# Performance work log

Hardware: AMD Instinct MI355X
Metric: run time of the kernel (lower is better)

## Reference

```python
import jax, jax.numpy as jnp
import numpy as np

N = 8192
IN_DIM = 256
HIDDEN = 128


def setup_inputs() -> dict:
    key = jax.random.key(0)
    k1, k2 = jax.random.split(key)
    X = jax.random.normal(k1, (N, IN_DIM), dtype=jnp.float32)
    # nn.Linear(in_dim, hidden, bias=False): weight [hidden, in_dim]
    W = jax.random.normal(k2, (HIDDEN, IN_DIM), dtype=jnp.float32) * (1.0 / np.sqrt(IN_DIM))
    return {"X": X, "W": W}


def reference(X, W):
    # Z = X @ W.T : [N, hidden]
    Z = jnp.einsum('ni,hi->nh', X, W)
    # Dense similarity graph: ReLU(Z Z^T), row-normalized
    A = jax.nn.relu(jnp.einsum('nh,mh->nm', Z, Z))  # [N, N]
    A = A / (A.sum(axis=-1, keepdims=True) + 1e-6)
    out = jnp.einsum('nm,mh->nh', A, Z)  # [N, hidden]
    return (out, A)
```

## Files before the change

### kernel.cpp

```cpp
#include <hip/hip_runtime.h>


#define NR 8192
#define KD 256
#define HD 128

typedef short v8s __attribute__((ext_vector_type(8)));
typedef float v4f __attribute__((ext_vector_type(4)));

static __device__ __forceinline__ ushort f2bf(float f) {
    union { float f; unsigned u; } c; c.f = f;
    unsigned u = c.u;
    u += 0x7fffu + ((u >> 16) & 1u);
    return (ushort)(u >> 16);
}
static __device__ __forceinline__ float bf2f(ushort b) {
    union { unsigned u; float f; } c; c.u = ((unsigned)b) << 16; return c.f;
}
static __device__ __forceinline__ unsigned pk2(float a, float b) {
    union { float f; unsigned u; } x, y; x.f = a; y.f = b;
    unsigned ua = x.u + 0x7fffu + ((x.u >> 16) & 1u);
    unsigned ub = y.u + 0x7fffu + ((y.u >> 16) & 1u);
    return (ua >> 16) | (ub & 0xffff0000u);
}

__global__ __launch_bounds__(256) void k_z(const float* __restrict__ X,
                                           const float* __restrict__ W,
                                           ushort* __restrict__ Zb,
                                           ushort* __restrict__ ZbT) {
    __shared__ ushort Xhi[16][264];
    __shared__ ushort Xlo[16][264];
    int tid = threadIdx.x, lane = tid & 63, wave = tid >> 6;
    int lm = lane & 15, lq = lane >> 4;
    int n0 = blockIdx.x * 16;
    int hbase = wave * 32;
    v8s Whi[2][8], Wlo[2][8];
#pragma unroll
    for (int hi = 0; hi < 2; ++hi) {
        const float* wp = W + (hbase + hi * 16 + lm) * KD + lq * 8;
#pragma unroll
        for (int ks = 0; ks < 8; ++ks) {
            float4 w0 = *(const float4*)(wp + ks * 32);
            float4 w1 = *(const float4*)(wp + ks * 32 + 4);
            float wv[8] = {w0.x, w0.y, w0.z, w0.w, w1.x, w1.y, w1.z, w1.w};
#pragma unroll
            for (int j = 0; j < 8; ++j) {
                ushort h = f2bf(wv[j]);
                Whi[hi][ks][j] = (short)h;
                Wlo[hi][ks][j] = (short)f2bf(wv[j] - bf2f(h));
            }
        }
    }
#pragma unroll
    for (int t = 0; t < 4; ++t) {
        int idx = tid + t * 256;
        int r = idx >> 6, c4 = (idx & 63) * 4;
        float4 x = *(const float4*)(X + (size_t)(n0 + r) * KD + c4);
        ushort h0 = f2bf(x.x), h1 = f2bf(x.y), h2 = f2bf(x.z), h3 = f2bf(x.w);
        unsigned a = ((unsigned)h0) | ((unsigned)h1 << 16);
        unsigned b = ((unsigned)h2) | ((unsigned)h3 << 16);
        unsigned c = ((unsigned)f2bf(x.x - bf2f(h0))) | ((unsigned)f2bf(x.y - bf2f(h1)) << 16);
        unsigned d = ((unsigned)f2bf(x.z - bf2f(h2))) | ((unsigned)f2bf(x.w - bf2f(h3)) << 16);
        *(uint2*)&Xhi[r][c4] = make_uint2(a, b);
        *(uint2*)&Xlo[r][c4] = make_uint2(c, d);
    }
    __syncthreads();
    {
        v8s Ah[8], Al[8];
#pragma unroll
        for (int ks = 0; ks < 8; ++ks) {
            Ah[ks] = *(const v8s*)&Xhi[lm][ks * 32 + lq * 8];
            Al[ks] = *(const v8s*)&Xlo[lm][ks * 32 + lq * 8];
        }
        v4f acc[2] = {{0.f, 0.f, 0.f, 0.f}, {0.f, 0.f, 0.f, 0.f}};
#pragma unroll
        for (int ks = 0; ks < 8; ++ks)
#pragma unroll
            for (int hi = 0; hi < 2; ++hi) {
                acc[hi] = __builtin_amdgcn_mfma_f32_16x16x32_bf16(Ah[ks], Whi[hi][ks], acc[hi], 0, 0, 0);
                acc[hi] = __builtin_amdgcn_mfma_f32_16x16x32_bf16(Ah[ks], Wlo[hi][ks], acc[hi], 0, 0, 0);
                acc[hi] = __builtin_amdgcn_mfma_f32_16x16x32_bf16(Al[ks], Whi[hi][ks], acc[hi], 0, 0, 0);
            }
#pragma unroll
        for (int hi = 0; hi < 2; ++hi) {
            int h = hbase + hi * 16 + lm;
            int nb = n0 + lq * 4;
            ushort b0 = f2bf(acc[hi][0]), b1 = f2bf(acc[hi][1]);
            ushort b2 = f2bf(acc[hi][2]), b3 = f2bf(acc[hi][3]);
            Zb[(size_t)(nb + 0) * HD + h] = b0;
            Zb[(size_t)(nb + 1) * HD + h] = b1;
            Zb[(size_t)(nb + 2) * HD + h] = b2;
            Zb[(size_t)(nb + 3) * HD + h] = b3;
            *(uint2*)&ZbT[(size_t)h * NR + nb] =
                make_uint2(((unsigned)b0) | ((unsigned)b1 << 16), ((unsigned)b2) | ((unsigned)b3 << 16));
        }
    }
}

__global__ __launch_bounds__(256) void k_rowsum(const ushort* __restrict__ Zb,
                                                float* __restrict__ rowsum) {
    __shared__ ushort ZC[2][64][136];
    int tid = threadIdx.x, lane = tid & 63, wave = tid >> 6;
    int lm = lane & 15, lq = lane >> 4;
    int rb = blockIdx.x >> 4, cs = blockIdx.x & 15;
    int row0 = rb * 128, cstart = cs * 512;
    v8s Bfr[2][4];
#pragma unroll
    for (int ri = 0; ri < 2; ++ri)
#pragma unroll
        for (int ks = 0; ks < 4; ++ks)
            Bfr[ri][ks] =
                *(const v8s*)(Zb + (size_t)(row0 + wave * 32 + ri * 16 + lm) * HD + ks * 32 + lq * 8);
    float rs[2] = {0.f, 0.f};
#pragma unroll
    for (int t = 0; t < 4; ++t) {
        int idx = tid + t * 256;
        int r = idx >> 4, c8 = (idx & 15) * 8;
        *(uint4*)&ZC[0][r][c8] = *(const uint4*)(Zb + (size_t)(cstart + r) * HD + c8);
    }
    __syncthreads();
    for (int it = 0; it < 8; ++it) {
        int cur = it & 1;
        int c0 = cstart + it * 64;
        uint4 sr[4];
        if (it < 7) {
#pragma unroll
            for (int t = 0; t < 4; ++t) {
                int idx = tid + t * 256;
                int r = idx >> 4, c8 = (idx & 15) * 8;
                sr[t] = *(const uint4*)(Zb + (size_t)(c0 + 64 + r) * HD + c8);
            }
        }
#pragma unroll
        for (int ci = 0; ci < 4; ++ci) {
            v8s Af[4];
#pragma unroll
            for (int ks = 0; ks < 4; ++ks)
                Af[ks] = *(const v8s*)&ZC[cur][ci * 16 + lm][ks * 32 + lq * 8];
            v4f a0 = {0.f, 0.f, 0.f, 0.f}, a1 = {0.f, 0.f, 0.f, 0.f};
#pragma unroll
            for (int ks = 0; ks < 4; ++ks) {
                a0 = __builtin_amdgcn_mfma_f32_16x16x32_bf16(Af[ks], Bfr[0][ks], a0, 0, 0, 0);
                a1 = __builtin_amdgcn_mfma_f32_16x16x32_bf16(Af[ks], Bfr[1][ks], a1, 0, 0, 0);
            }
            rs[0] += fmaxf(a0[0], 0.f) + fmaxf(a0[1], 0.f) + fmaxf(a0[2], 0.f) + fmaxf(a0[3], 0.f);
            rs[1] += fmaxf(a1[0], 0.f) + fmaxf(a1[1], 0.f) + fmaxf(a1[2], 0.f) + fmaxf(a1[3], 0.f);
        }
        if (it < 7) {
#pragma unroll
            for (int t = 0; t < 4; ++t) {
                int idx = tid + t * 256;
                int r = idx >> 4, c8 = (idx & 15) * 8;
                *(uint4*)&ZC[cur ^ 1][r][c8] = sr[t];
            }
        }
        __syncthreads();
    }
#pragma unroll
    for (int ri = 0; ri < 2; ++ri) {
        float v = rs[ri];
        v += __shfl_xor(v, 16, 64);
        v += __shfl_xor(v, 32, 64);
        if (lq == 0) atomicAdd(&rowsum[row0 + wave * 32 + ri * 16 + lm], v);
    }
}

__global__ __launch_bounds__(256) void k_main(const ushort* __restrict__ Zb,
                                              const ushort* __restrict__ ZbT,
                                              const float* __restrict__ rowsum,
                                              float* __restrict__ outp,
                                              float* __restrict__ Ap) {
    __shared__ ushort ZC[2][64][136];
    __shared__ ushort PT[2][64][72];
    int tid = threadIdx.x, lane = tid & 63, wave = tid >> 6;
    int lm = lane & 15, lq = lane >> 4;
    int rb = blockIdx.x >> 3, cs = blockIdx.x & 7;
    int row0 = rb * 64, colb = cs * 1024;
    int wr2 = wave >> 1, wc2 = wave & 1;
    v8s Bfr[2][4];
#pragma unroll
    for (int ri = 0; ri < 2; ++ri)
#pragma unroll
        for (int ks = 0; ks < 4; ++ks)
            Bfr[ri][ks] =
                *(const v8s*)(Zb + (size_t)(row0 + wr2 * 32 + ri * 16 + lm) * HD + ks * 32 + lq * 8);
    float rsv[2];
#pragma unroll
    for (int ri = 0; ri < 2; ++ri)
        rsv[ri] = 1.0f / (rowsum[row0 + wr2 * 32 + ri * 16 + lm] + 1e-6f);
    v4f U[2][4];
#pragma unroll
    for (int ri = 0; ri < 2; ++ri)
#pragma unroll
        for (int hi = 0; hi < 4; ++hi) U[ri][hi] = (v4f){0.f, 0.f, 0.f, 0.f};

#pragma unroll
    for (int t = 0; t < 4; ++t) {
        int idx = tid + t * 256;
        int r = idx >> 4, c8 = (idx & 15) * 8;
        *(uint4*)&ZC[0][r][c8] = *(const uint4*)(Zb + (size_t)(colb + r) * HD + c8);
    }
    __syncthreads();

    float* ap0 = Ap + (size_t)(row0 + wr2 * 32 + lm) * NR + colb + wc2 * 32 + lq * 4;
    float* ap1 = ap0 + (size_t)16 * NR;

    for (int it = 0; it < 16; ++it) {
        int cur = it & 1;
        int c0 = colb + it * 64;
        uint4 sr[4];
        if (it < 15) {
#pragma unroll
            for (int t = 0; t < 4; ++t) {
                int idx = tid + t * 256;
                int r = idx >> 4, c8 = (idx & 15) * 8;
                sr[t] = *(const uint4*)(Zb + (size_t)(c0 + 64 + r) * HD + c8);
            }
        }
        v8s Bz[4][2];
#pragma unroll
        for (int hi = 0; hi < 4; ++hi)
#pragma unroll
            for (int ks = 0; ks < 2; ++ks)
                Bz[hi][ks] = *(const v8s*)(ZbT + (size_t)(wc2 * 64 + hi * 16 + lm) * NR + c0 +
                                           ks * 32 + lq * 8);
        v4f avst[2][2];
#pragma unroll
        for (int ci = 0; ci < 2; ++ci) {
            v8s Af[4];
#pragma unroll
            for (int ks = 0; ks < 4; ++ks)
                Af[ks] = *(const v8s*)&ZC[cur][wc2 * 32 + ci * 16 + lm][ks * 32 + lq * 8];
            v4f S0 = {0.f, 0.f, 0.f, 0.f}, S1 = {0.f, 0.f, 0.f, 0.f};
#pragma unroll
            for (int ks = 0; ks < 4; ++ks) {
                S0 = __builtin_amdgcn_mfma_f32_16x16x32_bf16(Af[ks], Bfr[0][ks], S0, 0, 0, 0);
                S1 = __builtin_amdgcn_mfma_f32_16x16x32_bf16(Af[ks], Bfr[1][ks], S1, 0, 0, 0);
            }
            int cb = wc2 * 32 + ci * 16 + lq * 4;
            {
                v4f av;
                av[0] = fmaxf(S0[0], 0.f) * rsv[0]; av[1] = fmaxf(S0[1], 0.f) * rsv[0];
                av[2] = fmaxf(S0[2], 0.f) * rsv[0]; av[3] = fmaxf(S0[3], 0.f) * rsv[0];
                avst[ci][0] = av;
                *(uint2*)&PT[cur][wr2 * 32 + lm][cb] = make_uint2(pk2(av[0], av[1]), pk2(av[2], av[3]));
            }
            {
                v4f av;
                av[0] = fmaxf(S1[0], 0.f) * rsv[1]; av[1] = fmaxf(S1[1], 0.f) * rsv[1];
                av[2] = fmaxf(S1[2], 0.f) * rsv[1]; av[3] = fmaxf(S1[3], 0.f) * rsv[1];
                avst[ci][1] = av;
                *(uint2*)&PT[cur][wr2 * 32 + 16 + lm][cb] =
                    make_uint2(pk2(av[0], av[1]), pk2(av[2], av[3]));
            }
        }
        if (it < 15) {
#pragma unroll
            for (int t = 0; t < 4; ++t) {
                int idx = tid + t * 256;
                int r = idx >> 4, c8 = (idx & 15) * 8;
                *(uint4*)&ZC[cur ^ 1][r][c8] = sr[t];
            }
        }
        __syncthreads();
#pragma unroll
        for (int ci = 0; ci < 2; ++ci) {
            __builtin_nontemporal_store(avst[ci][0], (v4f*)(ap0 + ci * 16));
            __builtin_nontemporal_store(avst[ci][1], (v4f*)(ap1 + ci * 16));
        }
#pragma unroll
        for (int ks = 0; ks < 2; ++ks) {
            v8s P0 = *(const v8s*)&PT[cur][wr2 * 32 + lm][ks * 32 + lq * 8];
            v8s P1 = *(const v8s*)&PT[cur][wr2 * 32 + 16 + lm][ks * 32 + lq * 8];
#pragma unroll
            for (int hi = 0; hi < 4; ++hi) {
                U[0][hi] = __builtin_amdgcn_mfma_f32_16x16x32_bf16(P0, Bz[hi][ks], U[0][hi], 0, 0, 0);
                U[1][hi] = __builtin_amdgcn_mfma_f32_16x16x32_bf16(P1, Bz[hi][ks], U[1][hi], 0, 0, 0);
            }
        }
        ap0 += 64;
        ap1 += 64;
    }
#pragma unroll
    for (int ri = 0; ri < 2; ++ri)
#pragma unroll
        for (int hi = 0; hi < 4; ++hi)
#pragma unroll
            for (int j = 0; j < 4; ++j)
                atomicAdd(&outp[(size_t)(row0 + wr2 * 32 + ri * 16 + lq * 4 + j) * HD +
                                wc2 * 64 + hi * 16 + lm],
                          U[ri][hi][j]);
}

extern "C" void kernel_launch(void* const* d_in, const int* in_sizes, int n_in,
                              void* d_out, int out_size, void* d_ws, size_t ws_size,
                              hipStream_t stream) {
    (void)in_sizes; (void)n_in; (void)out_size; (void)ws_size;
    const float* X = (const float*)d_in[0];
    const float* W = (const float*)d_in[1];
    float* outp = (float*)d_out;
    float* Ap = outp + (size_t)NR * HD;
    char* ws = (char*)d_ws;
    ushort* Zb = (ushort*)ws;
    ushort* ZbT = (ushort*)(ws + (size_t)NR * HD * 2);
    float* rowsum = (float*)(ws + (size_t)NR * HD * 4);

    (void)hipMemsetAsync(outp, 0, (size_t)NR * HD * sizeof(float), stream);
    (void)hipMemsetAsync(rowsum, 0, NR * sizeof(float), stream);
    k_z<<<dim3(NR / 16), dim3(256), 0, stream>>>(X, W, Zb, ZbT);
    k_rowsum<<<dim3(1024), dim3(256), 0, stream>>>(Zb, rowsum);
    k_main<<<dim3(1024), dim3(256), 0, stream>>>(Zb, ZbT, rowsum, outp, Ap);
}
```

Measured before the change: 361.9 us.

## Fuse unnormalized relu(ZZ^T)Z into rowsum pass and split A write kernel

The rowsum kernel now also accumulates the unnormalized product relu(ZZ^T)·Z, since row normalization factors out of the final matmul. A small kernel then scales that product by the reciprocal rowsum. The A-writing kernel becomes a pure store-bound pass that reads Z tiles directly from global memory, with no LDS or second MFMA stage. This separates the compute-heavy work from the 256MB A write, at the cost of an extra Uacc buffer, an extra launch and more registers in the fused kernel.

```diff
diff --git a/kernel.cpp b/kernel.cpp
--- a/kernel.cpp
+++ b/kernel.cpp
@@ -97,13 +97,17 @@
     }
 }
 
-__global__ __launch_bounds__(256) void k_rowsum(const ushort* __restrict__ Zb,
-                                                float* __restrict__ rowsum) {
+__global__ __launch_bounds__(256, 2) void k_sv(const ushort* __restrict__ Zb,
+                                               const ushort* __restrict__ ZbT,
+                                               float* __restrict__ rowsum,
+                                               float* __restrict__ Uacc) {
     __shared__ ushort ZC[2][64][136];
+    __shared__ ushort PT[2][128][72];
     int tid = threadIdx.x, lane = tid & 63, wave = tid >> 6;
     int lm = lane & 15, lq = lane >> 4;
-    int rb = blockIdx.x >> 4, cs = blockIdx.x & 15;
-    int row0 = rb * 128, cstart = cs * 512;
+    int rb = blockIdx.x >> 3, cs = blockIdx.x & 7;
+    int row0 = rb * 128, cstart = cs * 1024;
+    int rh2 = wave >> 1, hh = wave & 1;
     v8s Bfr[2][4];
 #pragma unroll
     for (int ri = 0; ri < 2; ++ri)
@@ -112,6 +116,12 @@
             Bfr[ri][ks] =
                 *(const v8s*)(Zb + (size_t)(row0 + wave * 32 + ri * 16 + lm) * HD + ks * 32 + lq * 8);
     float rs[2] = {0.f, 0.f};
+    v4f U[4][4];
+#pragma unroll
+    for (int rA = 0; rA < 4; ++rA)
+#pragma unroll
+        for (int hi = 0; hi < 4; ++hi) U[rA][hi] = (v4f){0.f, 0.f, 0.f, 0.f};
+
 #pragma unroll
     for (int t = 0; t < 4; ++t) {
         int idx = tid + t * 256;
@@ -119,11 +129,12 @@
         *(uint4*)&ZC[0][r][c8] = *(const uint4*)(Zb + (size_t)(cstart + r) * HD + c8);
     }
     __syncthreads();
-    for (int it = 0; it < 8; ++it) {
+
+    for (int it = 0; it < 16; ++it) {
         int cur = it & 1;
         int c0 = cstart + it * 64;
         uint4 sr[4];
-        if (it < 7) {
+        if (it < 15) {
 #pragma unroll
             for (int t = 0; t < 4; ++t) {
                 int idx = tid + t * 256;
@@ -131,6 +142,13 @@
                 sr[t] = *(const uint4*)(Zb + (size_t)(c0 + 64 + r) * HD + c8);
             }
         }
+        v8s Bz[4][2];
+#pragma unroll
+        for (int hi = 0; hi < 4; ++hi)
+#pragma unroll
+            for (int ks = 0; ks < 2; ++ks)
+                Bz[hi][ks] = *(const v8s*)(ZbT + (size_t)(hh * 64 + hi * 16 + lm) * NR + c0 +
+                                           ks * 32 + lq * 8);
 #pragma unroll
         for (int ci = 0; ci < 4; ++ci) {
             v8s Af[4];
@@ -143,10 +161,21 @@
                 a0 = __builtin_amdgcn_mfma_f32_16x16x32_bf16(Af[ks], Bfr[0][ks], a0, 0, 0, 0);
                 a1 = __builtin_amdgcn_mfma_f32_16x16x32_bf16(Af[ks], Bfr[1][ks], a1, 0, 0, 0);
             }
-            rs[0] += fmaxf(a0[0], 0.f) + fmaxf(a0[1], 0.f) + fmaxf(a0[2], 0.f) + fmaxf(a0[3], 0.f);
-            rs[1] += fmaxf(a1[0], 0.f) + fmaxf(a1[1], 0.f) + fmaxf(a1[2], 0.f) + fmaxf(a1[3], 0.f);
-        }
-        if (it < 7) {
+            int cb = ci * 16 + lq * 4;
+            {
+                float f0 = fmaxf(a0[0], 0.f), f1 = fmaxf(a0[1], 0.f);
+                float f2 = fmaxf(a0[2], 0.f), f3 = fmaxf(a0[3], 0.f);
+                rs[0] += f0 + f1 + f2 + f3;
+                *(uint2*)&PT[cur][wave * 32 + lm][cb] = make_uint2(pk2(f0, f1), pk2(f2, f3));
+            }
+            {
+                float f0 = fmaxf(a1[0], 0.f), f1 = fmaxf(a1[1], 0.f);
+                float f2 = fmaxf(a1[2], 0.f), f3 = fmaxf(a1[3], 0.f);
+                rs[1] += f0 + f1 + f2 + f3;
+                *(uint2*)&PT[cur][wave * 32 + 16 + lm][cb] = make_uint2(pk2(f0, f1), pk2(f2, f3));
+            }
+        }
+        if (it < 15) {
 #pragma unroll
             for (int t = 0; t < 4; ++t) {
                 int idx = tid + t * 256;
@@ -155,6 +184,18 @@
             }
         }
         __syncthreads();
+#pragma unroll
+        for (int ks = 0; ks < 2; ++ks) {
+            v8s Pf[4];
+#pragma unroll
+            for (int rA = 0; rA < 4; ++rA)
+                Pf[rA] = *(const v8s*)&PT[cur][rh2 * 64 + rA * 16 + lm][ks * 32 + lq * 8];
+#pragma unroll
+            for (int hi = 0; hi < 4; ++hi)
+#pragma unroll
+                for (int rA = 0; rA < 4; ++rA)
+                    U[rA][hi] = __builtin_amdgcn_mfma_f32_16x16x32_bf16(Pf[rA], Bz[hi][ks], U[rA][hi], 0, 0, 0);
+        }
     }
 #pragma unroll
     for (int ri = 0; ri < 2; ++ri) {
@@ -163,19 +204,23 @@
         v += __shfl_xor(v, 32, 64);
         if (lq == 0) atomicAdd(&rowsum[row0 + wave * 32 + ri * 16 + lm], v);
     }
-}
-
-__global__ __launch_bounds__(256) void k_main(const ushort* __restrict__ Zb,
-                                              const ushort* __restrict__ ZbT,
+    float* ub = Uacc + (size_t)(row0 + rh2 * 64) * HD + hh * 64;
+#pragma unroll
+    for (int rA = 0; rA < 4; ++rA)
+#pragma unroll
+        for (int hi = 0; hi < 4; ++hi)
+#pragma unroll
+            for (int j = 0; j < 4; ++j)
+                atomicAdd(&ub[(size_t)(rA * 16 + lq * 4 + j) * HD + hi * 16 + lm], U[rA][hi][j]);
+}
+
+__global__ __launch_bounds__(256, 4) void k_a(const ushort* __restrict__ Zb,
                                               const float* __restrict__ rowsum,
-                                              float* __restrict__ outp,
                                               float* __restrict__ Ap) {
-    __shared__ ushort ZC[2][64][136];
-    __shared__ ushort PT[2][64][72];
     int tid = threadIdx.x, lane = tid & 63, wave = tid >> 6;
     int lm = lane & 15, lq = lane >> 4;
-    int rb = blockIdx.x >> 3, cs = blockIdx.x & 7;
-    int row0 = rb * 64, colb = cs * 1024;
+    int rb = blockIdx.x >> 4, cs = blockIdx.x & 15;
+    int row0 = rb * 64, colb = cs * 512;
     int wr2 = wave >> 1, wc2 = wave & 1;
     v8s Bfr[2][4];
 #pragma unroll
@@ -188,108 +233,46 @@
 #pragma unroll
     for (int ri = 0; ri < 2; ++ri)
         rsv[ri] = 1.0f / (rowsum[row0 + wr2 * 32 + ri * 16 + lm] + 1e-6f);
-    v4f U[2][4];
-#pragma unroll
-    for (int ri = 0; ri < 2; ++ri)
-#pragma unroll
-        for (int hi = 0; hi < 4; ++hi) U[ri][hi] = (v4f){0.f, 0.f, 0.f, 0.f};
-
-#pragma unroll
-    for (int t = 0; t < 4; ++t) {
-        int idx = tid + t * 256;
-        int r = idx >> 4, c8 = (idx & 15) * 8;
-        *(uint4*)&ZC[0][r][c8] = *(const uint4*)(Zb + (size_t)(colb + r) * HD + c8);
-    }
-    __syncthreads();
-
+    const ushort* afp = Zb + (size_t)(colb + wc2 * 32 + lm) * HD + lq * 8;
     float* ap0 = Ap + (size_t)(row0 + wr2 * 32 + lm) * NR + colb + wc2 * 32 + lq * 4;
     float* ap1 = ap0 + (size_t)16 * NR;
-
-    for (int it = 0; it < 16; ++it) {
-        int cur = it & 1;
-        int c0 = colb + it * 64;
-        uint4 sr[4];
-        if (it < 15) {
-#pragma unroll
-            for (int t = 0; t < 4; ++t) {
-                int idx = tid + t * 256;
-                int r = idx >> 4, c8 = (idx & 15) * 8;
-                sr[t] = *(const uint4*)(Zb + (size_t)(c0 + 64 + r) * HD + c8);
-            }
-        }
-        v8s Bz[4][2];
-#pragma unroll
-        for (int hi = 0; hi < 4; ++hi)
-#pragma unroll
-            for (int ks = 0; ks < 2; ++ks)
-                Bz[hi][ks] = *(const v8s*)(ZbT + (size_t)(wc2 * 64 + hi * 16 + lm) * NR + c0 +
-                                           ks * 32 + lq * 8);
-        v4f avst[2][2];
+    for (int it = 0; it < 8; ++it) {
 #pragma unroll
         for (int ci = 0; ci < 2; ++ci) {
             v8s Af[4];
 #pragma unroll
             for (int ks = 0; ks < 4; ++ks)
-                Af[ks] = *(const v8s*)&ZC[cur][wc2 * 32 + ci * 16 + lm][ks * 32 + lq * 8];
+                Af[ks] = *(const v8s*)(afp + (size_t)(ci * 16) * HD + ks * 32);
             v4f S0 = {0.f, 0.f, 0.f, 0.f}, S1 = {0.f, 0.f, 0.f, 0.f};
 #pragma unroll
             for (int ks = 0; ks < 4; ++ks) {
                 S0 = __builtin_amdgcn_mfma_f32_16x16x32_bf16(Af[ks], Bfr[0][ks], S0, 0, 0, 0);
                 S1 = __builtin_amdgcn_mfma_f32_16x16x32_bf16(Af[ks], Bfr[1][ks], S1, 0, 0, 0);
             }
-            int cb = wc2 * 32 + ci * 16 + lq * 4;
-            {
-                v4f av;
-                av[0] = fmaxf(S0[0], 0.f) * rsv[0]; av[1] = fmaxf(S0[1], 0.f) * rsv[0];
-                av[2] = fmaxf(S0[2], 0.f) * rsv[0]; av[3] = fmaxf(S0[3], 0.f) * rsv[0];
-                avst[ci][0] = av;
-                *(uint2*)&PT[cur][wr2 * 32 + lm][cb] = make_uint2(pk2(av[0], av[1]), pk2(av[2], av[3]));
-            }
-            {
-                v4f av;
-                av[0] = fmaxf(S1[0], 0.f) * rsv[1]; av[1] = fmaxf(S1[1], 0.f) * rsv[1];
-                av[2] = fmaxf(S1[2], 0.f) * rsv[1]; av[3] = fmaxf(S1[3], 0.f) * rsv[1];
-                avst[ci][1] = av;
-                *(uint2*)&PT[cur][wr2 * 32 + 16 + lm][cb] =
-                    make_uint2(pk2(av[0], av[1]), pk2(av[2], av[3]));
-            }
-        }
-        if (it < 15) {
-#pragma unroll
-            for (int t = 0; t < 4; ++t) {
-                int idx = tid + t * 256;
-                int r = idx >> 4, c8 = (idx & 15) * 8;
-                *(uint4*)&ZC[cur ^ 1][r][c8] = sr[t];
-            }
-        }
-        __syncthreads();
-#pragma unroll
-        for (int ci = 0; ci < 2; ++ci) {
-            __builtin_nontemporal_store(avst[ci][0], (v4f*)(ap0 + ci * 16));
-            __builtin_nontemporal_store(avst[ci][1], (v4f*)(ap1 + ci * 16));
-        }
-#pragma unroll
-        for (int ks = 0; ks < 2; ++ks) {
-            v8s P0 = *(const v8s*)&PT[cur][wr2 * 32 + lm][ks * 32 + lq * 8];
-            v8s P1 = *(const v8s*)&PT[cur][wr2 * 32 + 16 + lm][ks * 32 + lq * 8];
-#pragma unroll
-            for (int hi = 0; hi < 4; ++hi) {
-                U[0][hi] = __builtin_amdgcn_mfma_f32_16x16x32_bf16(P0, Bz[hi][ks], U[0][hi], 0, 0, 0);
-                U[1][hi] = __builtin_amdgcn_mfma_f32_16x16x32_bf16(P1, Bz[hi][ks], U[1][hi], 0, 0, 0);
-            }
-        }
+            v4f av;
+            av[0] = fmaxf(S0[0], 0.f) * rsv[0]; av[1] = fmaxf(S0[1], 0.f) * rsv[0];
+            av[2] = fmaxf(S0[2], 0.f) * rsv[0]; av[3] = fmaxf(S0[3], 0.f) * rsv[0];
+            __builtin_nontemporal_store(av, (v4f*)(ap0 + ci * 16));
+            av[0] = fmaxf(S1[0], 0.f) * rsv[1]; av[1] = fmaxf(S1[1], 0.f) * rsv[1];
+            av[2] = fmaxf(S1[2], 0.f) * rsv[1]; av[3] = fmaxf(S1[3], 0.f) * rsv[1];
+            __builtin_nontemporal_store(av, (v4f*)(ap1 + ci * 16));
+        }
+        afp += (size_t)64 * HD;
         ap0 += 64;
         ap1 += 64;
     }
-#pragma unroll
-    for (int ri = 0; ri < 2; ++ri)
-#pragma unroll
-        for (int hi = 0; hi < 4; ++hi)
-#pragma unroll
-            for (int j = 0; j < 4; ++j)
-                atomicAdd(&outp[(size_t)(row0 + wr2 * 32 + ri * 16 + lq * 4 + j) * HD +
-                                wc2 * 64 + hi * 16 + lm],
-                          U[ri][hi][j]);
+}
+
+__global__ __launch_bounds__(256) void k_out(const float* __restrict__ Uacc,
+                                             const float* __restrict__ rowsum,
+                                             float* __restrict__ outp) {
+    int idx = blockIdx.x * 256 + threadIdx.x;
+    int r = idx >> 5, h4 = (idx & 31) * 4;
+    float rsv = 1.0f / (rowsum[r] + 1e-6f);
+    size_t o = (size_t)r * HD + h4;
+    float4 v = *(const float4*)(Uacc + o);
+    float4 s = make_float4(v.x * rsv, v.y * rsv, v.z * rsv, v.w * rsv);
+    *(float4*)(outp + o) = s;
 }
 
 extern "C" void kernel_launch(void* const* d_in, const int* in_sizes, int n_in,
@@ -304,10 +287,12 @@
     ushort* Zb = (ushort*)ws;
     ushort* ZbT = (ushort*)(ws + (size_t)NR * HD * 2);
     float* rowsum = (float*)(ws + (size_t)NR * HD * 4);
-
-    (void)hipMemsetAsync(outp, 0, (size_t)NR * HD * sizeof(float), stream);
+    float* Uacc = (float*)(ws + (size_t)NR * HD * 4 + NR * 4);
+
     (void)hipMemsetAsync(rowsum, 0, NR * sizeof(float), stream);
+    (void)hipMemsetAsync(Uacc, 0, (size_t)NR * HD * sizeof(float), stream);
     k_z<<<dim3(NR / 16), dim3(256), 0, stream>>>(X, W, Zb, ZbT);
-    k_rowsum<<<dim3(1024), dim3(256), 0, stream>>>(Zb, rowsum);
-    k_main<<<dim3(1024), dim3(256), 0, stream>>>(Zb, ZbT, rowsum, outp, Ap);
-}
+    k_sv<<<dim3(512), dim3(256), 0, stream>>>(Zb, ZbT, rowsum, Uacc);
+    k_a<<<dim3(2048), dim3(256), 0, stream>>>(Zb, rowsum, Ap);
+    k_out<<<dim3(1024), dim3(256), 0, stream>>>(Uacc, rowsum, outp);
+}
```

After: 386.7 us. 6.8% more time.
